# Kernel tuning notes

Hardware: AMD Instinct MI355X
Metric: run time of the kernel (lower is better)

The kernel has to match this reference:

```python
import jax, jax.numpy as jnp
import numpy as np

B, S, H = 1024, 100, 256          # users(batch), seq_len, hidden
L, U = 20000, 20000               # location_size, user_size
EL, EU = 500000, 400000           # nnz of loc-loc and user-loc sparse graphs
LAMBDA_T, LAMBDA_S = 0.1, 1000.0
DAY = 86400.0


def setup_inputs() -> dict:
    key = jax.random.key(0)
    k = jax.random.split(key, 20)
    sd = 1.0 / np.sqrt(H)
    full_seq = jax.random.randint(k[0], (B, S), 0, L)
    full_seq_map = jax.random.randint(k[1], (B, S), 0, L)
    length = jax.random.randint(k[2], (B,), 1, S + 1)  # >=1 so mask never empty
    user_id = jax.random.randint(k[3], (B,), 0, U)
    time_delta = jax.random.uniform(k[4], (B, S), dtype=jnp.float32) * DAY
    geo_delta = jax.random.uniform(k[5], (B, S), dtype=jnp.float32) * 1e-3
    enc_emb = jax.random.normal(k[6], (L, H), dtype=jnp.float32) * sd
    user_emb = jax.random.normal(k[7], (U, H), dtype=jnp.float32) * sd
    emb2 = jax.random.normal(k[8], (L, H), dtype=jnp.float32) * sd  # embed_layer table
    # loc-loc random-walk graph (row-normalized weights), COO edge list
    row_loc = jax.random.randint(k[9], (EL,), 0, L)
    col_loc = jax.random.randint(k[10], (EL,), 0, L)
    vals_loc = jax.random.uniform(k[11], (EL,), dtype=jnp.float32) / (EL / L)
    # user-loc interact graph (row-normalized), COO edge list
    row_usr = jax.random.randint(k[12], (EU,), 0, U)
    col_usr = jax.random.randint(k[13], (EU,), 0, L)
    vals_usr = jax.random.uniform(k[14], (EU,), dtype=jnp.float32) / (EU / U)
    W_ih = jax.random.normal(k[15], (H, H), dtype=jnp.float32) * sd
    W_hh = jax.random.normal(k[16], (H, H), dtype=jnp.float32) * sd
    b_ih = jnp.zeros((H,), jnp.float32)
    b_hh = jnp.zeros((H,), jnp.float32)
    W1 = jax.random.normal(k[17], (L, 3 * H), dtype=jnp.float32) * sd  # source declares 2H but feeds 3H concat
    b1 = jnp.zeros((L,), jnp.float32)
    h0 = jax.random.normal(k[18], (B, H), dtype=jnp.float32) * (1.0 / H)  # per-user random init state
    return dict(full_seq=full_seq, full_seq_map=full_seq_map, length=length,
                user_id=user_id, time_delta=time_delta, geo_delta=geo_delta,
                enc_emb=enc_emb, user_emb=user_emb, emb2=emb2,
                row_loc=row_loc, col_loc=col_loc, vals_loc=vals_loc,
                row_usr=row_usr, col_usr=col_usr, vals_usr=vals_usr,
                W_ih=W_ih, W_hh=W_hh, b_ih=b_ih, b_hh=b_hh, W1=W1, b1=b1, h0=h0)


def reference(full_seq, full_seq_map, length, user_id, time_delta, geo_delta,
              enc_emb, user_emb, emb2, row_loc, col_loc, vals_loc,
              row_usr, col_usr, vals_usr, W_ih, W_hh, b_ih, b_hh, W1, b1, h0):
    # sparse.mm(graph, loc_emb): one random-walk propagation over locations
    encoder_weight = jax.ops.segment_sum(vals_loc[:, None] * enc_emb[col_loc],
                                         row_loc, num_segments=L)  # [L,H]
    x_emb = encoder_weight[full_seq_map]                           # [B,S,H]
    # sparse.mm(interact_graph, loc_emb): user preference from visited locations
    ew_user = jax.ops.segment_sum(vals_usr[:, None] * enc_emb[col_usr],
                                  row_usr, num_segments=U)         # [U,H]
    user_pref = ew_user[user_id][:, None, :]                       # [B,1,H]
    user_loc_sim = jnp.exp(-jnp.linalg.norm(user_pref - x_emb, axis=-1))  # [B,S]
    # vanilla tanh RNN (batch_first), scan over time
    def step(h, x_t):
        h = jnp.tanh(x_t @ W_ih.T + b_ih + h @ W_hh.T + b_hh)
        return h, h
    _, outs = jax.lax.scan(step, h0, jnp.swapaxes(x_emb, 0, 1))    # [S,B,H]
    out = jnp.swapaxes(outs, 0, 1)                                 # [B,S,H]
    # temporal / spatial decay weights
    a_j = (jnp.cos(time_delta * 2 * np.pi / DAY) + 1) / 2 * jnp.exp(-(time_delta / DAY * LAMBDA_T))
    b_j = jnp.exp(-geo_delta * LAMBDA_S)
    w_j = (a_j * b_j + 1e-10) * user_loc_sim
    mask = (length[:, None] > jnp.arange(S)[None, :]).astype(w_j.dtype)
    w_j = w_j * mask                                               # [B,S]
    denom = jnp.sum(w_j, axis=1, keepdims=True)                    # [B,1]
    out_w = jnp.sum(out * w_j[..., None], axis=1) / denom          # [B,H]
    x2 = emb2[full_seq]                                            # embed_layer (dropout=eval)
    out_w2 = jnp.sum(x2 * w_j[..., None], axis=1) / denom          # [B,H]
    p_u = user_emb[user_id]                                        # [B,H]
    feat = jnp.concatenate([out_w, p_u, out_w2], axis=1)           # [B,3H]
    return feat @ W1.T + b1                                        # [B,L]
```

## Files before the change

kernel.cpp:

```cpp
#include <hip/hip_runtime.h>
#include <math.h>

#define B_  1024
#define S_  100
#define H_  256
#define L_  20000
#define U_  20000
#define EL_ 500000
#define EU_ 400000

typedef __bf16 bf16x8 __attribute__((ext_vector_type(8)));
typedef __bf16 bf16x4 __attribute__((ext_vector_type(4)));
typedef float  f32x4  __attribute__((ext_vector_type(4)));
typedef _Float16 f16x8 __attribute__((ext_vector_type(8)));

__global__ void k_mark(const int* __restrict__ uid, int* __restrict__ flags) {
    int i = blockIdx.x * blockDim.x + threadIdx.x;
    if (i < B_) flags[uid[i]] = 1;
}

__global__ void k_hist2(const int* __restrict__ rowL, const int* __restrict__ rowU,
                        const int* __restrict__ flags,
                        int* __restrict__ cntL, int* __restrict__ cntU) {
    int e = blockIdx.x * blockDim.x + threadIdx.x;
    if (e < EL_) {
        atomicAdd(&cntL[rowL[e]], 1);
    } else if (e < EL_ + EU_) {
        int r = rowU[e - EL_];
        if (flags[r]) atomicAdd(&cntU[r], 1);
    }
}

__global__ __launch_bounds__(1024) void k_scan2(const int* __restrict__ cntA,
                                                int* __restrict__ offsA, int* __restrict__ curA,
                                                const int* __restrict__ cntB,
                                                int* __restrict__ offsB, int* __restrict__ curB) {
    const int* cnt = blockIdx.x ? cntB : cntA;
    int* offs      = blockIdx.x ? offsB : offsA;
    int* cursor    = blockIdx.x ? curB : curA;
    __shared__ int wsum[16];
    __shared__ int carry_s;
    int tid = threadIdx.x;
    int lane = tid & 63, wv = tid >> 6;
    if (tid == 0) carry_s = 0;
    __syncthreads();
    for (int base = 0; base < L_; base += 1024) {
        int v = (base + tid < L_) ? cnt[base + tid] : 0;
        int x = v;
#pragma unroll
        for (int off = 1; off < 64; off <<= 1) {
            int y = __shfl_up(x, off, 64);
            if (lane >= off) x += y;
        }
        if (lane == 63) wsum[wv] = x;
        __syncthreads();
        if (wv == 0) {
            int s = (lane < 16) ? wsum[lane] : 0;
#pragma unroll
            for (int off = 1; off < 16; off <<= 1) {
                int y = __shfl_up(s, off, 64);
                if (lane >= off) s += y;
            }
            if (lane < 16) wsum[lane] = s;
        }
        __syncthreads();
        int excl = x - v + (wv ? wsum[wv - 1] : 0) + carry_s;
        if (base + tid < L_) { offs[base + tid] = excl; cursor[base + tid] = excl; }
        __syncthreads();
        if (tid == 0) carry_s += wsum[15];
        __syncthreads();
    }
    if (tid == 0) offs[L_] = carry_s;
}

__global__ void k_place2(const int* __restrict__ rowL, const int* __restrict__ colL,
                         const float* __restrict__ valL, int* __restrict__ curL,
                         int* __restrict__ colLs, float* __restrict__ valLs,
                         const int* __restrict__ rowU, const int* __restrict__ colU,
                         const float* __restrict__ valU, const int* __restrict__ flags,
                         int* __restrict__ curU, int* __restrict__ colUs,
                         float* __restrict__ valUs) {
    int e = blockIdx.x * blockDim.x + threadIdx.x;
    if (e < EL_) {
        int pos = atomicAdd(&curL[rowL[e]], 1);
        colLs[pos] = colL[e];
        valLs[pos] = valL[e];
    } else if (e < EL_ + EU_) {
        int e2 = e - EL_;
        int r = rowU[e2];
        if (!flags[r]) return;
        int pos = atomicAdd(&curU[r], 1);
        colUs[pos] = colU[e2];
        valUs[pos] = valU[e2];
    }
}

__global__ __launch_bounds__(256) void k_gather2(
        const int* __restrict__ offsL, const int* __restrict__ colLs,
        const float* __restrict__ valLs, float* __restrict__ encw,
        const int* __restrict__ offsU, const int* __restrict__ colUs,
        const float* __restrict__ valUs, float* __restrict__ ewu,
        const int* __restrict__ flags, const float* __restrict__ emb) {
    int r = blockIdx.x;
    const int* offs; const int* col_s; const float* val_s; float* out;
    if (r < L_) {
        offs = offsL; col_s = colLs; val_s = valLs; out = encw;
    } else {
        r -= L_;
        if (!flags[r]) return;
        offs = offsU; col_s = colUs; val_s = valUs; out = ewu;
    }
    int tid = threadIdx.x;
    int lo = offs[r], hi = offs[r + 1];
    float acc = 0.f;
    int i = lo;
    for (; i + 1 < hi; i += 2) {
        int c0 = col_s[i], c1 = col_s[i + 1];
        float v0 = val_s[i], v1 = val_s[i + 1];
        float e0 = emb[(long long)c0 * H_ + tid];
        float e1 = emb[(long long)c1 * H_ + tid];
        acc += v0 * e0 + v1 * e1;
    }
    if (i < hi) acc += val_s[i] * emb[(long long)col_s[i] * H_ + tid];
    out[(long long)r * H_ + tid] = acc;
}

#define BM 128
#define BN 128
#define BK 16
#define PADW 132

__global__ __launch_bounds__(256) void k_gemm(
        const float* __restrict__ A, const float* __restrict__ Bm,
        const float* __restrict__ bias1, const float* __restrict__ bias2,
        float* __restrict__ C, int M, int N, int K) {
    __shared__ float As[BK][PADW];
    __shared__ float Bs[BK][PADW];
    int m0 = blockIdx.x * BM;
    int n0 = blockIdx.y * BN;
    int tid = threadIdx.x;
    int tn = tid & 15, tm = tid >> 4;

    float acc[8][8];
#pragma unroll
    for (int i = 0; i < 8; i++)
#pragma unroll
        for (int j = 0; j < 8; j++) acc[i][j] = 0.f;

    for (int k0 = 0; k0 < K; k0 += BK) {
#pragma unroll
        for (int h = 0; h < 2; h++) {
            int v = tid + h * 256;
            int rw = v >> 2, c4 = v & 3;
            int ar = m0 + rw; if (ar > M - 1) ar = M - 1;
            float4 a = *(const float4*)(A + (long long)ar * K + k0 + c4 * 4);
            As[c4 * 4 + 0][rw] = a.x; As[c4 * 4 + 1][rw] = a.y;
            As[c4 * 4 + 2][rw] = a.z; As[c4 * 4 + 3][rw] = a.w;
            int br = n0 + rw; if (br > N - 1) br = N - 1;
            float4 b = *(const float4*)(Bm + (long long)br * K + k0 + c4 * 4);
            Bs[c4 * 4 + 0][rw] = b.x; Bs[c4 * 4 + 1][rw] = b.y;
            Bs[c4 * 4 + 2][rw] = b.z; Bs[c4 * 4 + 3][rw] = b.w;
        }
        __syncthreads();
#pragma unroll
        for (int kk = 0; kk < BK; kk++) {
            float4 a0 = *(const float4*)&As[kk][tm * 8];
            float4 a1 = *(const float4*)&As[kk][tm * 8 + 4];
            float4 b0 = *(const float4*)&Bs[kk][tn * 8];
            float4 b1 = *(const float4*)&Bs[kk][tn * 8 + 4];
            float av[8] = {a0.x, a0.y, a0.z, a0.w, a1.x, a1.y, a1.z, a1.w};
            float bv[8] = {b0.x, b0.y, b0.z, b0.w, b1.x, b1.y, b1.z, b1.w};
#pragma unroll
            for (int i = 0; i < 8; i++)
#pragma unroll
                for (int j = 0; j < 8; j++) acc[i][j] += av[i] * bv[j];
        }
        __syncthreads();
    }

    float bsum[8];
#pragma unroll
    for (int j = 0; j < 8; j++) {
        int n = n0 + tn * 8 + j;
        float bb = 0.f;
        if (n < N) {
            if (bias1) bb += bias1[n];
            if (bias2) bb += bias2[n];
        }
        bsum[j] = bb;
    }
#pragma unroll
    for (int i = 0; i < 8; i++) {
        int m = m0 + tm * 8 + i;
        if (m < M) {
#pragma unroll
            for (int j = 0; j < 8; j++) {
                int n = n0 + tn * 8 + j;
                if (n < N) C[(long long)m * N + n] = acc[i][j] + bsum[j];
            }
        }
    }
}

__global__ __launch_bounds__(256) void k_cvt(const float4* __restrict__ src,
                                             bf16x4* __restrict__ dst, int n4) {
    int i = blockIdx.x * blockDim.x + threadIdx.x;
    if (i >= n4) return;
    float4 v = src[i];
    bf16x4 o;
    o[0] = (__bf16)v.x; o[1] = (__bf16)v.y; o[2] = (__bf16)v.z; o[3] = (__bf16)v.w;
    dst[i] = o;
}

__global__ __launch_bounds__(256) void k_gemm_bf16(
        const __bf16* __restrict__ A, const __bf16* __restrict__ Bw,
        const float* __restrict__ bias, float* __restrict__ C,
        int M, int N, int K) {
    __shared__ __bf16 Asl[128 * 32];
    __shared__ __bf16 Bsl[128 * 32];
    int tid = threadIdx.x;
    int lane = tid & 63, w = tid >> 6;
    int wm = w >> 1, wn = w & 1;
    int m0 = blockIdx.x * 128, n0 = blockIdx.y * 128;

    f32x4 acc[4][4];
#pragma unroll
    for (int i = 0; i < 4; i++)
#pragma unroll
        for (int j = 0; j < 4; j++) acc[i][j] = (f32x4){0.f, 0.f, 0.f, 0.f};

    int fm = lane & 15, fq = lane >> 4;

    for (int k0 = 0; k0 < K; k0 += 32) {
#pragma unroll
        for (int h = 0; h < 2; h++) {
            int c = h * 256 + w * 64 + lane;
            int r = c >> 2, qsw = c & 3;
            int q = qsw ^ ((r >> 1) & 3);
            const __bf16* gA = A + (long long)(m0 + r) * K + k0 + q * 8;
            __builtin_amdgcn_global_load_lds(
                (const __attribute__((address_space(1))) void*)gA,
                (__attribute__((address_space(3))) void*)(Asl + (h * 256 + w * 64) * 8),
                16, 0, 0);
            int br = n0 + r; if (br > N - 1) br = N - 1;
            const __bf16* gB = Bw + (long long)br * K + k0 + q * 8;
            __builtin_amdgcn_global_load_lds(
                (const __attribute__((address_space(1))) void*)gB,
                (__attribute__((address_space(3))) void*)(Bsl + (h * 256 + w * 64) * 8),
                16, 0, 0);
        }
        __syncthreads();

        bf16x8 af[4], bfr[4];
#pragma unroll
        for (int mi = 0; mi < 4; mi++) {
            int r = wm * 64 + mi * 16 + fm;
            int ch = r * 4 + (fq ^ ((r >> 1) & 3));
            af[mi] = *(const bf16x8*)(Asl + ch * 8);
        }
#pragma unroll
        for (int ni = 0; ni < 4; ni++) {
            int r = wn * 64 + ni * 16 + fm;
            int ch = r * 4 + (fq ^ ((r >> 1) & 3));
            bfr[ni] = *(const bf16x8*)(Bsl + ch * 8);
        }
#pragma unroll
        for (int mi = 0; mi < 4; mi++)
#pragma unroll
            for (int ni = 0; ni < 4; ni++)
                acc[mi][ni] = __builtin_amdgcn_mfma_f32_16x16x32_bf16(
                    af[mi], bfr[ni], acc[mi][ni], 0, 0, 0);
        __syncthreads();
    }

#pragma unroll
    for (int ni = 0; ni < 4; ni++) {
        int col = n0 + wn * 64 + ni * 16 + fm;
        if (col >= N) continue;
        float bb = bias[col];
#pragma unroll
        for (int mi = 0; mi < 4; mi++) {
            int row = m0 + wm * 64 + mi * 16 + fq * 4;
#pragma unroll
            for (int r = 0; r < 4; r++)
                C[(long long)(row + r) * N + col] = acc[mi][ni][r] + bb;
        }
    }
}

__global__ __launch_bounds__(256) void k_simwj(
        const int* __restrict__ map, const int* __restrict__ length, const int* __restrict__ uid,
        const float* __restrict__ td_, const float* __restrict__ gd_,
        const float* __restrict__ encw, const float* __restrict__ ewu,
        float* __restrict__ wj, float* __restrict__ denom) {
    int b = blockIdx.x;
    __shared__ float up[H_];
    __shared__ float wjl[S_];
    int tid = threadIdx.x;
    int u = uid[b];
    up[tid] = ewu[(long long)u * H_ + tid];
    __syncthreads();
    int wv = tid >> 6, lane = tid & 63;
    int len = length[b];
    for (int s = wv; s < S_; s += 4) {
        int mi = map[b * S_ + s];
        float4 x = ((const float4*)(encw + (long long)mi * H_))[lane];
        float4 uu = *(const float4*)&up[lane * 4];
        float dx = uu.x - x.x, dy = uu.y - x.y, dz = uu.z - x.z, dw = uu.w - x.w;
        float d2 = dx * dx + dy * dy + dz * dz + dw * dw;
#pragma unroll
        for (int off = 32; off; off >>= 1) d2 += __shfl_xor(d2, off, 64);
        if (lane == 0) {
            float nrm = sqrtf(d2);
            float sim = expf(-nrm);
            float td = td_[b * S_ + s], gd = gd_[b * S_ + s];
            float aj = (cosf(td * 7.27220521664304e-05f) + 1.0f) * 0.5f *
                       expf(-td * 1.1574074074074073e-06f);
            float bj = expf(-gd * 1000.0f);
            float w = (aj * bj + 1e-10f) * sim;
            if (s >= len) w = 0.f;
            wjl[s] = w;
            wj[b * S_ + s] = w;
        }
    }
    __syncthreads();
    if (tid < 64) {
        float v = (tid < S_) ? wjl[tid] : 0.f;
        if (tid + 64 < S_) v += wjl[tid + 64];
#pragma unroll
        for (int off = 32; off; off >>= 1) v += __shfl_xor(v, off, 64);
        if (tid == 0) denom[b] = v;
    }
}

#define RNN_STRIDE 264

__global__ __launch_bounds__(1024, 1) void k_rnn_mfma(
        const float* __restrict__ EWW, const float* __restrict__ Whh,
        const int* __restrict__ map, const float* __restrict__ wj,
        const float* __restrict__ h0g, float* __restrict__ out_acc) {
    __shared__ _Float16 hbuf[2][16 * RNN_STRIDE];
    __shared__ int   maps_s[S_ * 16];
    __shared__ float wjs_s[S_ * 16];

    int tid = threadIdx.x;
    int lane = tid & 63, w = tid >> 6;
    int fm = lane & 15, fq = lane >> 4;
    int b0 = blockIdx.x * 16;
    int col = w * 16 + fm;

    for (int i = tid; i < 16 * S_; i += 1024) {
        int m = i / S_, s = i - m * S_;
        maps_s[s * 16 + m] = map[(b0 + m) * S_ + s];
        wjs_s[s * 16 + m] = wj[(b0 + m) * S_ + s];
    }
    if (tid < 256) {
        int m = tid >> 4, seg = tid & 15;
        const float4* src = (const float4*)(h0g + (long long)(b0 + m) * H_ + seg * 16);
        float4 a = src[0], bq = src[1], cq = src[2], dq = src[3];
        f16x8 v0, v1;
        v0[0] = (_Float16)a.x;  v0[1] = (_Float16)a.y;  v0[2] = (_Float16)a.z;  v0[3] = (_Float16)a.w;
        v0[4] = (_Float16)bq.x; v0[5] = (_Float16)bq.y; v0[6] = (_Float16)bq.z; v0[7] = (_Float16)bq.w;
        v1[0] = (_Float16)cq.x; v1[1] = (_Float16)cq.y; v1[2] = (_Float16)cq.z; v1[3] = (_Float16)cq.w;
        v1[4] = (_Float16)dq.x; v1[5] = (_Float16)dq.y; v1[6] = (_Float16)dq.z; v1[7] = (_Float16)dq.w;
        *(f16x8*)(hbuf[0] + m * RNN_STRIDE + seg * 16) = v0;
        *(f16x8*)(hbuf[0] + m * RNN_STRIDE + seg * 16 + 8) = v1;
    }

    f16x8 wf[8];
    {
        const float* wrow = Whh + (long long)col * H_;
#pragma unroll
        for (int c = 0; c < 8; c++) {
            int k = c * 32 + fq * 8;
            float4 p = *(const float4*)(wrow + k);
            float4 q = *(const float4*)(wrow + k + 4);
            f16x8 v;
            v[0] = (_Float16)p.x; v[1] = (_Float16)p.y; v[2] = (_Float16)p.z; v[3] = (_Float16)p.w;
            v[4] = (_Float16)q.x; v[5] = (_Float16)q.y; v[6] = (_Float16)q.z; v[7] = (_Float16)q.w;
            wf[c] = v;
        }
    }

    float accv[4];
#pragma unroll
    for (int r = 0; r < 4; r++) accv[r] = 0.f;

    __syncthreads();

    float xc[4], xn[4];
#pragma unroll
    for (int r = 0; r < 4; r++)
        xc[r] = EWW[(long long)maps_s[0 * 16 + fq * 4 + r] * H_ + col];

    for (int s = 0; s < S_; s++) {
        const _Float16* hr = hbuf[s & 1];
        _Float16*       hw = hbuf[(s + 1) & 1];

        f32x4 acc = (f32x4){xc[0], xc[1], xc[2], xc[3]};

        if (s + 1 < S_) {
#pragma unroll
            for (int r = 0; r < 4; r++)
                xn[r] = EWW[(long long)maps_s[(s + 1) * 16 + fq * 4 + r] * H_ + col];
        }

        f16x8 af[8];
#pragma unroll
        for (int c = 0; c < 8; c++)
            af[c] = *(const f16x8*)(hr + fm * RNN_STRIDE + c * 32 + fq * 8);
#pragma unroll
        for (int c = 0; c < 8; c++)
            acc = __builtin_amdgcn_mfma_f32_16x16x32_f16(af[c], wf[c], acc, 0, 0, 0);

#pragma unroll
        for (int r = 0; r < 4; r++) {
            float t = acc[r];
            t = fminf(15.f, fmaxf(-15.f, t));
            float e = __expf(2.f * t);
            float hv = 1.f - 2.f / (e + 1.f);
            accv[r] += wjs_s[s * 16 + fq * 4 + r] * hv;
            hw[(fq * 4 + r) * RNN_STRIDE + col] = (_Float16)hv;
        }

        __syncthreads();

#pragma unroll
        for (int r = 0; r < 4; r++) xc[r] = xn[r];
    }

#pragma unroll
    for (int r = 0; r < 4; r++)
        out_acc[(long long)(b0 + fq * 4 + r) * H_ + col] = accv[r];
}

__global__ __launch_bounds__(256) void k_feat(
        const float* __restrict__ out_acc, const float* __restrict__ denom,
        const int* __restrict__ uid, const float* __restrict__ user_emb,
        const int* __restrict__ seq, const float* __restrict__ wj,
        const float* __restrict__ emb2, __bf16* __restrict__ featb) {
    int b = blockIdx.x, j = threadIdx.x;
    __shared__ float wjl[S_];
    __shared__ int sq[S_];
    if (j < S_) {
        wjl[j] = wj[b * S_ + j];
        sq[j] = seq[b * S_ + j];
    }
    __syncthreads();
    float inv = 1.f / denom[b];
    featb[(long long)b * 768 + j] = (__bf16)(out_acc[(long long)b * H_ + j] * inv);
    featb[(long long)b * 768 + 256 + j] = (__bf16)(user_emb[(long long)uid[b] * H_ + j]);
    float a2 = 0.f;
    for (int s = 0; s < S_; s++) a2 += wjl[s] * emb2[(long long)sq[s] * H_ + j];
    featb[(long long)b * 768 + 512 + j] = (__bf16)(a2 * inv);
}

extern "C" void kernel_launch(void* const* d_in, const int* in_sizes, int n_in,
                              void* d_out, int out_size, void* d_ws, size_t ws_size,
                              hipStream_t stream) {
    const int*   full_seq     = (const int*)d_in[0];
    const int*   full_seq_map = (const int*)d_in[1];
    const int*   length       = (const int*)d_in[2];
    const int*   user_id      = (const int*)d_in[3];
    const float* time_delta   = (const float*)d_in[4];
    const float* geo_delta    = (const float*)d_in[5];
    const float* enc_emb      = (const float*)d_in[6];
    const float* user_emb     = (const float*)d_in[7];
    const float* emb2         = (const float*)d_in[8];
    const int*   row_loc      = (const int*)d_in[9];
    const int*   col_loc      = (const int*)d_in[10];
    const float* vals_loc     = (const float*)d_in[11];
    const int*   row_usr      = (const int*)d_in[12];
    const int*   col_usr      = (const int*)d_in[13];
    const float* vals_usr     = (const float*)d_in[14];
    const float* W_ih         = (const float*)d_in[15];
    const float* W_hh         = (const float*)d_in[16];
    const float* b_ih         = (const float*)d_in[17];
    const float* b_hh         = (const float*)d_in[18];
    const float* W1           = (const float*)d_in[19];
    const float* b1           = (const float*)d_in[20];
    const float* h0g          = (const float*)d_in[21];
    float* out = (float*)d_out;

    float* ws = (float*)d_ws;
    size_t o = 0;
    int*   flags = (int*)(ws + o); o += U_;
    float* ewu   = ws + o; o += (size_t)U_ * H_;
    float* encw  = ws + o; o += (size_t)L_ * H_;
    float* EWW   = ws + o; o += (size_t)L_ * H_;
    size_t late_base = o;
    float* wj    = ws + o; o += (size_t)B_ * S_;
    float* denom = ws + o; o += B_;
    float* oacc  = ws + o; o += (size_t)B_ * H_;
    size_t a = o;
    int*   cntL  = (int*)(ws + a); a += L_ + 1;
    int*   offsL = (int*)(ws + a); a += L_ + 1;
    int*   curL  = (int*)(ws + a); a += L_ + 1;
    int*   colLs = (int*)(ws + a); a += EL_;
    float* valLs = ws + a;         a += EL_;
    int*   cntU  = (int*)EWW;
    int*   offsU = cntU + (U_ + 1);
    int*   curU  = offsU + (U_ + 1);
    int*   colUs = curU + (U_ + 1);
    float* valUs = (float*)(colUs + EU_);
    __bf16* w1bf   = (__bf16*)ws;
    __bf16* featbf = (__bf16*)EWW;

    hipMemsetAsync(flags, 0, U_ * sizeof(int), stream);
    hipMemsetAsync(cntL, 0, (L_ + 1) * sizeof(int), stream);
    hipMemsetAsync(cntU, 0, (U_ + 1) * sizeof(int), stream);
    k_mark<<<(B_ + 255) / 256, 256, 0, stream>>>(user_id, flags);

    k_hist2<<<(EL_ + EU_ + 255) / 256, 256, 0, stream>>>(row_loc, row_usr, flags, cntL, cntU);
    k_scan2<<<2, 1024, 0, stream>>>(cntL, offsL, curL, cntU, offsU, curU);
    k_place2<<<(EL_ + EU_ + 255) / 256, 256, 0, stream>>>(
        row_loc, col_loc, vals_loc, curL, colLs, valLs,
        row_usr, col_usr, vals_usr, flags, curU, colUs, valUs);
    k_gather2<<<L_ + U_, 256, 0, stream>>>(offsL, colLs, valLs, encw,
                                           offsU, colUs, valUs, ewu, flags, enc_emb);

    k_gemm<<<dim3((L_ + BM - 1) / BM, (H_ + BN - 1) / BN), 256, 0, stream>>>(
        encw, W_ih, b_ih, b_hh, EWW, L_, H_, H_);
    k_simwj<<<B_, 256, 0, stream>>>(full_seq_map, length, user_id, time_delta,
                                    geo_delta, encw, ewu, wj, denom);
    k_rnn_mfma<<<B_ / 16, 1024, 0, stream>>>(EWW, W_hh, full_seq_map, wj, h0g, oacc);
    k_feat<<<B_, 256, 0, stream>>>(oacc, denom, user_id, user_emb, full_seq, wj, emb2, featbf);

    k_cvt<<<((L_ * 3 * H_ / 4) + 255) / 256, 256, 0, stream>>>(
        (const float4*)W1, (bf16x4*)w1bf, L_ * 3 * H_ / 4);

    k_gemm_bf16<<<dim3(B_ / 128, (L_ + 127) / 128), 256, 0, stream>>>(
        featbf, w1bf, b1, out, B_, L_, 3 * H_);
}
```

Measured before the change: 654.7 us.

## Store graph-embedding intermediates in fp16 and run W_ih projection on MFMA

The sparse-gather outputs (encw, ewu) and the projected table EWW are now stored as fp16 instead of fp32, halving their write and read traffic in simwj and the RNN. The scalar fp32 tiled GEMM for encw·W_ih^T is replaced by a templated fp16 MFMA GEMM, after a small conversion of W_ih to fp16. The final W1 GEMM also switches from bf16 to fp16 MFMA. fp16 has less range than bf16 or fp32, so precision and overflow risk rise slightly, and there is one extra conversion kernel.

Result: faster. 608.6 us (-7.0%).

```diff
diff --git a/kernel.cpp b/kernel.cpp
--- a/kernel.cpp
+++ b/kernel.cpp
@@ -9,10 +9,9 @@
 #define EL_ 500000
 #define EU_ 400000
 
-typedef __bf16 bf16x8 __attribute__((ext_vector_type(8)));
-typedef __bf16 bf16x4 __attribute__((ext_vector_type(4)));
 typedef float  f32x4  __attribute__((ext_vector_type(4)));
 typedef _Float16 f16x8 __attribute__((ext_vector_type(8)));
+typedef _Float16 f16x4 __attribute__((ext_vector_type(4)));
 
 __global__ void k_mark(const int* __restrict__ uid, int* __restrict__ flags) {
     int i = blockIdx.x * blockDim.x + threadIdx.x;
@@ -97,18 +96,18 @@
 
 __global__ __launch_bounds__(256) void k_gather2(
         const int* __restrict__ offsL, const int* __restrict__ colLs,
-        const float* __restrict__ valLs, float* __restrict__ encw,
+        const float* __restrict__ valLs, _Float16* __restrict__ encwh,
         const int* __restrict__ offsU, const int* __restrict__ colUs,
-        const float* __restrict__ valUs, float* __restrict__ ewu,
+        const float* __restrict__ valUs, _Float16* __restrict__ ewuh,
         const int* __restrict__ flags, const float* __restrict__ emb) {
     int r = blockIdx.x;
-    const int* offs; const int* col_s; const float* val_s; float* out;
+    const int* offs; const int* col_s; const float* val_s; _Float16* out;
     if (r < L_) {
-        offs = offsL; col_s = colLs; val_s = valLs; out = encw;
+        offs = offsL; col_s = colLs; val_s = valLs; out = encwh;
     } else {
         r -= L_;
         if (!flags[r]) return;
-        offs = offsU; col_s = colUs; val_s = valUs; out = ewu;
+        offs = offsU; col_s = colUs; val_s = valUs; out = ewuh;
     }
     int tid = threadIdx.x;
     int lo = offs[r], hi = offs[r + 1];
@@ -122,102 +121,26 @@
         acc += v0 * e0 + v1 * e1;
     }
     if (i < hi) acc += val_s[i] * emb[(long long)col_s[i] * H_ + tid];
-    out[(long long)r * H_ + tid] = acc;
-}
-
-#define BM 128
-#define BN 128
-#define BK 16
-#define PADW 132
-
-__global__ __launch_bounds__(256) void k_gemm(
-        const float* __restrict__ A, const float* __restrict__ Bm,
-        const float* __restrict__ bias1, const float* __restrict__ bias2,
-        float* __restrict__ C, int M, int N, int K) {
-    __shared__ float As[BK][PADW];
-    __shared__ float Bs[BK][PADW];
-    int m0 = blockIdx.x * BM;
-    int n0 = blockIdx.y * BN;
-    int tid = threadIdx.x;
-    int tn = tid & 15, tm = tid >> 4;
-
-    float acc[8][8];
-#pragma unroll
-    for (int i = 0; i < 8; i++)
-#pragma unroll
-        for (int j = 0; j < 8; j++) acc[i][j] = 0.f;
-
-    for (int k0 = 0; k0 < K; k0 += BK) {
-#pragma unroll
-        for (int h = 0; h < 2; h++) {
-            int v = tid + h * 256;
-            int rw = v >> 2, c4 = v & 3;
-            int ar = m0 + rw; if (ar > M - 1) ar = M - 1;
-            float4 a = *(const float4*)(A + (long long)ar * K + k0 + c4 * 4);
-            As[c4 * 4 + 0][rw] = a.x; As[c4 * 4 + 1][rw] = a.y;
-            As[c4 * 4 + 2][rw] = a.z; As[c4 * 4 + 3][rw] = a.w;
-            int br = n0 + rw; if (br > N - 1) br = N - 1;
-            float4 b = *(const float4*)(Bm + (long long)br * K + k0 + c4 * 4);
-            Bs[c4 * 4 + 0][rw] = b.x; Bs[c4 * 4 + 1][rw] = b.y;
-            Bs[c4 * 4 + 2][rw] = b.z; Bs[c4 * 4 + 3][rw] = b.w;
-        }
-        __syncthreads();
-#pragma unroll
-        for (int kk = 0; kk < BK; kk++) {
-            float4 a0 = *(const float4*)&As[kk][tm * 8];
-            float4 a1 = *(const float4*)&As[kk][tm * 8 + 4];
-            float4 b0 = *(const float4*)&Bs[kk][tn * 8];
-            float4 b1 = *(const float4*)&Bs[kk][tn * 8 + 4];
-            float av[8] = {a0.x, a0.y, a0.z, a0.w, a1.x, a1.y, a1.z, a1.w};
-            float bv[8] = {b0.x, b0.y, b0.z, b0.w, b1.x, b1.y, b1.z, b1.w};
-#pragma unroll
-            for (int i = 0; i < 8; i++)
-#pragma unroll
-                for (int j = 0; j < 8; j++) acc[i][j] += av[i] * bv[j];
-        }
-        __syncthreads();
-    }
-
-    float bsum[8];
-#pragma unroll
-    for (int j = 0; j < 8; j++) {
-        int n = n0 + tn * 8 + j;
-        float bb = 0.f;
-        if (n < N) {
-            if (bias1) bb += bias1[n];
-            if (bias2) bb += bias2[n];
-        }
-        bsum[j] = bb;
-    }
-#pragma unroll
-    for (int i = 0; i < 8; i++) {
-        int m = m0 + tm * 8 + i;
-        if (m < M) {
-#pragma unroll
-            for (int j = 0; j < 8; j++) {
-                int n = n0 + tn * 8 + j;
-                if (n < N) C[(long long)m * N + n] = acc[i][j] + bsum[j];
-            }
-        }
-    }
-}
-
-__global__ __launch_bounds__(256) void k_cvt(const float4* __restrict__ src,
-                                             bf16x4* __restrict__ dst, int n4) {
+    out[(long long)r * H_ + tid] = (_Float16)acc;
+}
+
+__global__ __launch_bounds__(256) void k_cvth(const float4* __restrict__ src,
+                                              f16x4* __restrict__ dst, int n4) {
     int i = blockIdx.x * blockDim.x + threadIdx.x;
     if (i >= n4) return;
     float4 v = src[i];
-    bf16x4 o;
-    o[0] = (__bf16)v.x; o[1] = (__bf16)v.y; o[2] = (__bf16)v.z; o[3] = (__bf16)v.w;
+    f16x4 o;
+    o[0] = (_Float16)v.x; o[1] = (_Float16)v.y; o[2] = (_Float16)v.z; o[3] = (_Float16)v.w;
     dst[i] = o;
 }
 
-__global__ __launch_bounds__(256) void k_gemm_bf16(
-        const __bf16* __restrict__ A, const __bf16* __restrict__ Bw,
-        const float* __restrict__ bias, float* __restrict__ C,
-        int M, int N, int K) {
-    __shared__ __bf16 Asl[128 * 32];
-    __shared__ __bf16 Bsl[128 * 32];
+template <typename TO>
+__global__ __launch_bounds__(256) void k_gemm_mfma(
+        const _Float16* __restrict__ A, const _Float16* __restrict__ Bw,
+        const float* __restrict__ bias1, const float* __restrict__ bias2,
+        TO* __restrict__ C, int M, int N, int K) {
+    __shared__ _Float16 Asl[128 * 32];
+    __shared__ _Float16 Bsl[128 * 32];
     int tid = threadIdx.x;
     int lane = tid & 63, w = tid >> 6;
     int wm = w >> 1, wn = w & 1;
@@ -237,13 +160,13 @@
             int c = h * 256 + w * 64 + lane;
             int r = c >> 2, qsw = c & 3;
             int q = qsw ^ ((r >> 1) & 3);
-            const __bf16* gA = A + (long long)(m0 + r) * K + k0 + q * 8;
+            const _Float16* gA = A + (long long)(m0 + r) * K + k0 + q * 8;
             __builtin_amdgcn_global_load_lds(
                 (const __attribute__((address_space(1))) void*)gA,
                 (__attribute__((address_space(3))) void*)(Asl + (h * 256 + w * 64) * 8),
                 16, 0, 0);
             int br = n0 + r; if (br > N - 1) br = N - 1;
-            const __bf16* gB = Bw + (long long)br * K + k0 + q * 8;
+            const _Float16* gB = Bw + (long long)br * K + k0 + q * 8;
             __builtin_amdgcn_global_load_lds(
                 (const __attribute__((address_space(1))) void*)gB,
                 (__attribute__((address_space(3))) void*)(Bsl + (h * 256 + w * 64) * 8),
@@ -251,24 +174,24 @@
         }
         __syncthreads();
 
-        bf16x8 af[4], bfr[4];
+        f16x8 af[4], bfr[4];
 #pragma unroll
         for (int mi = 0; mi < 4; mi++) {
             int r = wm * 64 + mi * 16 + fm;
             int ch = r * 4 + (fq ^ ((r >> 1) & 3));
-            af[mi] = *(const bf16x8*)(Asl + ch * 8);
+            af[mi] = *(const f16x8*)(Asl + ch * 8);
         }
 #pragma unroll
         for (int ni = 0; ni < 4; ni++) {
             int r = wn * 64 + ni * 16 + fm;
             int ch = r * 4 + (fq ^ ((r >> 1) & 3));
-            bfr[ni] = *(const bf16x8*)(Bsl + ch * 8);
+            bfr[ni] = *(const f16x8*)(Bsl + ch * 8);
         }
 #pragma unroll
         for (int mi = 0; mi < 4; mi++)
 #pragma unroll
             for (int ni = 0; ni < 4; ni++)
-                acc[mi][ni] = __builtin_amdgcn_mfma_f32_16x16x32_bf16(
+                acc[mi][ni] = __builtin_amdgcn_mfma_f32_16x16x32_f16(
                     af[mi], bfr[ni], acc[mi][ni], 0, 0, 0);
         __syncthreads();
     }
@@ -277,13 +200,14 @@
     for (int ni = 0; ni < 4; ni++) {
         int col = n0 + wn * 64 + ni * 16 + fm;
         if (col >= N) continue;
-        float bb = bias[col];
+        float bb = bias1 ? bias1[col] : 0.f;
+        if (bias2) bb += bias2[col];
 #pragma unroll
         for (int mi = 0; mi < 4; mi++) {
             int row = m0 + wm * 64 + mi * 16 + fq * 4;
 #pragma unroll
             for (int r = 0; r < 4; r++)
-                C[(long long)(row + r) * N + col] = acc[mi][ni][r] + bb;
+                C[(long long)(row + r) * N + col] = (TO)(acc[mi][ni][r] + bb);
         }
     }
 }
@@ -291,22 +215,23 @@
 __global__ __launch_bounds__(256) void k_simwj(
         const int* __restrict__ map, const int* __restrict__ length, const int* __restrict__ uid,
         const float* __restrict__ td_, const float* __restrict__ gd_,
-        const float* __restrict__ encw, const float* __restrict__ ewu,
+        const _Float16* __restrict__ encwh, const _Float16* __restrict__ ewuh,
         float* __restrict__ wj, float* __restrict__ denom) {
     int b = blockIdx.x;
     __shared__ float up[H_];
     __shared__ float wjl[S_];
     int tid = threadIdx.x;
     int u = uid[b];
-    up[tid] = ewu[(long long)u * H_ + tid];
+    up[tid] = (float)ewuh[(long long)u * H_ + tid];
     __syncthreads();
     int wv = tid >> 6, lane = tid & 63;
     int len = length[b];
     for (int s = wv; s < S_; s += 4) {
         int mi = map[b * S_ + s];
-        float4 x = ((const float4*)(encw + (long long)mi * H_))[lane];
+        f16x4 xr = *(const f16x4*)(encwh + (long long)mi * H_ + lane * 4);
         float4 uu = *(const float4*)&up[lane * 4];
-        float dx = uu.x - x.x, dy = uu.y - x.y, dz = uu.z - x.z, dw = uu.w - x.w;
+        float dx = uu.x - (float)xr[0], dy = uu.y - (float)xr[1];
+        float dz = uu.z - (float)xr[2], dw = uu.w - (float)xr[3];
         float d2 = dx * dx + dy * dy + dz * dz + dw * dw;
 #pragma unroll
         for (int off = 32; off; off >>= 1) d2 += __shfl_xor(d2, off, 64);
@@ -336,7 +261,7 @@
 #define RNN_STRIDE 264
 
 __global__ __launch_bounds__(1024, 1) void k_rnn_mfma(
-        const float* __restrict__ EWW, const float* __restrict__ Whh,
+        const _Float16* __restrict__ EWWh, const float* __restrict__ Whh,
         const int* __restrict__ map, const float* __restrict__ wj,
         const float* __restrict__ h0g, float* __restrict__ out_acc) {
     __shared__ _Float16 hbuf[2][16 * RNN_STRIDE];
@@ -391,7 +316,7 @@
     float xc[4], xn[4];
 #pragma unroll
     for (int r = 0; r < 4; r++)
-        xc[r] = EWW[(long long)maps_s[0 * 16 + fq * 4 + r] * H_ + col];
+        xc[r] = (float)EWWh[(long long)maps_s[0 * 16 + fq * 4 + r] * H_ + col];
 
     for (int s = 0; s < S_; s++) {
         const _Float16* hr = hbuf[s & 1];
@@ -402,7 +327,7 @@
         if (s + 1 < S_) {
 #pragma unroll
             for (int r = 0; r < 4; r++)
-                xn[r] = EWW[(long long)maps_s[(s + 1) * 16 + fq * 4 + r] * H_ + col];
+                xn[r] = (float)EWWh[(long long)maps_s[(s + 1) * 16 + fq * 4 + r] * H_ + col];
         }
 
         f16x8 af[8];
@@ -438,7 +363,7 @@
         const float* __restrict__ out_acc, const float* __restrict__ denom,
         const int* __restrict__ uid, const float* __restrict__ user_emb,
         const int* __restrict__ seq, const float* __restrict__ wj,
-        const float* __restrict__ emb2, __bf16* __restrict__ featb) {
+        const float* __restrict__ emb2, _Float16* __restrict__ feath) {
     int b = blockIdx.x, j = threadIdx.x;
     __shared__ float wjl[S_];
     __shared__ int sq[S_];
@@ -448,11 +373,11 @@
     }
     __syncthreads();
     float inv = 1.f / denom[b];
-    featb[(long long)b * 768 + j] = (__bf16)(out_acc[(long long)b * H_ + j] * inv);
-    featb[(long long)b * 768 + 256 + j] = (__bf16)(user_emb[(long long)uid[b] * H_ + j]);
+    feath[(long long)b * 768 + j] = (_Float16)(out_acc[(long long)b * H_ + j] * inv);
+    feath[(long long)b * 768 + 256 + j] = (_Float16)(user_emb[(long long)uid[b] * H_ + j]);
     float a2 = 0.f;
     for (int s = 0; s < S_; s++) a2 += wjl[s] * emb2[(long long)sq[s] * H_ + j];
-    featb[(long long)b * 768 + 512 + j] = (__bf16)(a2 * inv);
+    feath[(long long)b * 768 + 512 + j] = (_Float16)(a2 * inv);
 }
 
 extern "C" void kernel_launch(void* const* d_in, const int* in_sizes, int n_in,
@@ -484,27 +409,27 @@
 
     float* ws = (float*)d_ws;
     size_t o = 0;
-    int*   flags = (int*)(ws + o); o += U_;
-    float* ewu   = ws + o; o += (size_t)U_ * H_;
-    float* encw  = ws + o; o += (size_t)L_ * H_;
-    float* EWW   = ws + o; o += (size_t)L_ * H_;
-    size_t late_base = o;
+    int*      flags = (int*)(ws + o);      o += U_;
+    _Float16* ewuh  = (_Float16*)(ws + o); o += (size_t)U_ * H_ / 2;
+    _Float16* encwh = (_Float16*)(ws + o); o += (size_t)L_ * H_ / 2;
+    _Float16* ewwh  = (_Float16*)(ws + o); o += (size_t)L_ * H_ / 2;
     float* wj    = ws + o; o += (size_t)B_ * S_;
     float* denom = ws + o; o += B_;
     float* oacc  = ws + o; o += (size_t)B_ * H_;
+    _Float16* feath = (_Float16*)(ws + o); o += (size_t)B_ * 3 * H_ / 2;
+    _Float16* wihh  = (_Float16*)(ws + o); o += (size_t)H_ * H_ / 2;
     size_t a = o;
-    int*   cntL  = (int*)(ws + a); a += L_ + 1;
-    int*   offsL = (int*)(ws + a); a += L_ + 1;
-    int*   curL  = (int*)(ws + a); a += L_ + 1;
+    int*   cntL  = (int*)(ws + a); a += L_ + 4;
+    int*   offsL = (int*)(ws + a); a += L_ + 4;
+    int*   curL  = (int*)(ws + a); a += L_ + 4;
     int*   colLs = (int*)(ws + a); a += EL_;
     float* valLs = ws + a;         a += EL_;
-    int*   cntU  = (int*)EWW;
-    int*   offsU = cntU + (U_ + 1);
-    int*   curU  = offsU + (U_ + 1);
-    int*   colUs = curU + (U_ + 1);
+    int*   cntU  = (int*)ewwh;
+    int*   offsU = cntU + (U_ + 4);
+    int*   curU  = offsU + (U_ + 4);
+    int*   colUs = curU + (U_ + 4);
     float* valUs = (float*)(colUs + EU_);
-    __bf16* w1bf   = (__bf16*)ws;
-    __bf16* featbf = (__bf16*)EWW;
+    _Float16* w1h = (_Float16*)ws;
 
     hipMemsetAsync(flags, 0, U_ * sizeof(int), stream);
     hipMemsetAsync(cntL, 0, (L_ + 1) * sizeof(int), stream);
@@ -516,19 +441,22 @@
     k_place2<<<(EL_ + EU_ + 255) / 256, 256, 0, stream>>>(
         row_loc, col_loc, vals_loc, curL, colLs, valLs,
         row_usr, col_usr, vals_usr, flags, curU, colUs, valUs);
-    k_gather2<<<L_ + U_, 256, 0, stream>>>(offsL, colLs, valLs, encw,
-                                           offsU, colUs, valUs, ewu, flags, enc_emb);
-
-    k_gemm<<<dim3((L_ + BM - 1) / BM, (H_ + BN - 1) / BN), 256, 0, stream>>>(
-        encw, W_ih, b_ih, b_hh, EWW, L_, H_, H_);
+    k_gather2<<<L_ + U_, 256, 0, stream>>>(offsL, colLs, valLs, encwh,
+                                           offsU, colUs, valUs, ewuh, flags, enc_emb);
+
+    k_cvth<<<((H_ * H_ / 4) + 255) / 256, 256, 0, stream>>>(
+        (const float4*)W_ih, (f16x4*)wihh, H_ * H_ / 4);
+    k_gemm_mfma<_Float16><<<dim3((L_ + 127) / 128, H_ / 128), 256, 0, stream>>>(
+        encwh, wihh, b_ih, b_hh, ewwh, L_, H_, H_);
+
     k_simwj<<<B_, 256, 0, stream>>>(full_seq_map, length, user_id, time_delta,
-                                    geo_delta, encw, ewu, wj, denom);
-    k_rnn_mfma<<<B_ / 16, 1024, 0, stream>>>(EWW, W_hh, full_seq_map, wj, h0g, oacc);
-    k_feat<<<B_, 256, 0, stream>>>(oacc, denom, user_id, user_emb, full_seq, wj, emb2, featbf);
-
-    k_cvt<<<((L_ * 3 * H_ / 4) + 255) / 256, 256, 0, stream>>>(
-        (const float4*)W1, (bf16x4*)w1bf, L_ * 3 * H_ / 4);
-
-    k_gemm_bf16<<<dim3(B_ / 128, (L_ + 127) / 128), 256, 0, stream>>>(
-        featbf, w1bf, b1, out, B_, L_, 3 * H_);
-}
+                                    geo_delta, encwh, ewuh, wj, denom);
+    k_rnn_mfma<<<B_ / 16, 1024, 0, stream>>>(ewwh, W_hh, full_seq_map, wj, h0g, oacc);
+    k_feat<<<B_, 256, 0, stream>>>(oacc, denom, user_id, user_emb, full_seq, wj, emb2, feath);
+
+    k_cvth<<<((L_ * 3 * H_ / 4) + 255) / 256, 256, 0, stream>>>(
+        (const float4*)W1, (f16x4*)w1h, L_ * 3 * H_ / 4);
+
+    k_gemm_mfma<float><<<dim3(B_ / 128, (L_ + 127) / 128), 256, 0, stream>>>(
+        feath, w1h, b1, nullptr, out, B_, L_, 3 * H_);
+}
```
